# Optimization experiments

Hardware: AMD Instinct MI355X
Metric: run time of the kernel (lower is better)

## Reference

```python
import jax, jax.numpy as jnp
from jax import lax
import numpy as np

B, IMG, PS = 64, 384, 16
DM, DS, DI = 96, 16, 96
DT_RANK = 6
NREP = 4
NCLS = 5
HP = IMG // PS            # 24 patches per side
N = HP * HP               # 576 tokens


def _ln(x, g, b):
    m = x.mean(-1, keepdims=True)
    v = ((x - m) ** 2).mean(-1, keepdims=True)
    return (x - m) * lax.rsqrt(v + 1e-5) * g + b


def setup_inputs() -> dict:
    key = jax.random.key(0)
    ks = jax.random.split(key, 16)
    nrm = lambda k, s: jax.random.normal(k, s, jnp.float32) * 0.02
    return {
        "x": jax.random.uniform(ks[0], (B, 3, IMG, IMG), jnp.float32),
        "W_pe": nrm(ks[1], (DM, 3, PS, PS)), "b_pe": jnp.zeros((DM,), jnp.float32),
        "W_vis": nrm(ks[2], (DM, 1)), "b_vis": jnp.zeros((1,), jnp.float32),
        "dn_g": jnp.ones((DM,), jnp.float32), "dn_b": jnp.zeros((DM,), jnp.float32),
        "W_gate": nrm(ks[3], (DM, DM)), "b_gate": jnp.zeros((DM,), jnp.float32),
        "ln_g": jnp.ones((DM,), jnp.float32), "ln_b": jnp.zeros((DM,), jnp.float32),
        "W_in": nrm(ks[4], (DM, 2 * DI)),
        "conv_w": nrm(ks[5], (DI, 1, 3)),
        "W_xproj": nrm(ks[6], (DI, DT_RANK + 2 * DS)),
        "W_dt": nrm(ks[7], (DT_RANK, DI)), "b_dt": jnp.full((DI,), -2.0, jnp.float32),
        "A_log": jnp.log(jnp.tile(jnp.arange(1, DS + 1, dtype=jnp.float32), (DI, 1))),
        "D": jnp.ones((DI,), jnp.float32),
        "W_out": nrm(ks[8], (DI, DM)),
        "hd_dw": nrm(ks[9], (DM, 1, 3, 3)),
        "bn_g": jnp.ones((DM,), jnp.float32), "bn_b": jnp.zeros((DM,), jnp.float32),
        "bn_m": jnp.zeros((DM,), jnp.float32), "bn_v": jnp.ones((DM,), jnp.float32),
        "W_heat": nrm(ks[10], (NCLS, DM)), "b_heat": jnp.full((NCLS,), -2.19, jnp.float32),
        "W_off": nrm(ks[11], (2, DM)), "b_off": jnp.zeros((2,), jnp.float32),
        "W_size": nrm(ks[12], (2, DM)), "b_size": jnp.zeros((2,), jnp.float32),
    }


def _forward(x, W_pe, b_pe, W_vis, b_vis, dn_g, dn_b, W_gate, b_gate,
             ln_g, ln_b, W_in, conv_w, W_xproj, W_dt, b_dt, A_log, D, W_out,
             hd_dw, bn_g, bn_b, bn_m, bn_v, W_heat, b_heat, W_off, b_off, W_size, b_size):
    # --- retinex preprocessing (single-scale, log domain) ---
    kblur = jnp.ones((3, 1, 5, 5), jnp.float32) / 25.0
    L = lax.conv_general_dilated(x, kblur, (1, 1), 'SAME',
                                 feature_group_count=3,
                                 dimension_numbers=('NCHW', 'OIHW', 'NCHW'))
    x = jnp.log1p(jnp.clip(x, 0.0)) - jnp.log1p(jnp.clip(L, 0.0))
    # --- patch embedding: strided conv -> tokens (B,N,DM) ---
    t = lax.conv_general_dilated(x, W_pe, (PS, PS), 'VALID',
                                 dimension_numbers=('NCHW', 'OIHW', 'NCHW'))
    t = t + b_pe[None, :, None, None]
    tokens = t.reshape(B, DM, N).transpose(0, 2, 1)
    # --- visibility estimator: per-token gate (B,N,1) ---
    vis = jax.nn.sigmoid(tokens @ W_vis + b_vis)
    # --- dual norm: LN + sigmoid gate ---
    tokens = _ln(tokens, dn_g, dn_b)
    norm_gate = jax.nn.sigmoid(tokens @ W_gate + b_gate)  # (B,N,DM)
    # --- weight-shared NC-SSM blocks ---
    A = -jnp.exp(A_log)  # (DI,DS)
    for _ in range(NREP):
        resid = tokens
        h = _ln(tokens, ln_g, ln_b)
        xz = h @ W_in                      # (B,N,2*DI)
        xin, z = xz[..., :DI], xz[..., DI:]
        # causal depthwise conv1d over sequence, kernel 3
        xc = xin.transpose(0, 2, 1)        # (B,DI,N)
        xc = lax.conv_general_dilated(xc, conv_w, (1,), [(2, 0)],
                                      feature_group_count=DI,
                                      dimension_numbers=('NCH', 'OIH', 'NCH'))
        xs = jax.nn.silu(xc.transpose(0, 2, 1))  # (B,N,DI)
        # selective-scan parameters
        proj = xs @ W_xproj                # (B,N,DT_RANK+2*DS)
        dt_raw = proj[..., :DT_RANK]
        Bc = proj[..., DT_RANK:DT_RANK + DS]
        Cc = proj[..., DT_RANK + DS:]
        dt = jax.nn.softplus(dt_raw @ W_dt + b_dt)  # (B,N,DI)
        # time-major scan
        def step(hst, inp):
            dt_t, B_t, C_t, x_t = inp      # (B,DI),(B,DS),(B,DS),(B,DI)
            dA = jnp.exp(dt_t[:, :, None] * A)                 # (B,DI,DS)
            hst = dA * hst + (dt_t * x_t)[:, :, None] * B_t[:, None, :]
            y = jnp.einsum('bds,bs->bd', hst, C_t)
            return hst, y
        h0 = jnp.zeros((B, DI, DS), jnp.float32)
        _, ys = lax.scan(step, h0, (dt.transpose(1, 0, 2), Bc.transpose(1, 0, 2),
                                    Cc.transpose(1, 0, 2), xs.transpose(1, 0, 2)))
        y = ys.transpose(1, 0, 2) + D * xs           # (B,N,DI)
        y = y * jax.nn.silu(z) * vis                  # gated by z and visibility
        tokens = resid + (y @ W_out) * norm_gate
    # --- CenterNet-style head ---
    f = tokens.transpose(0, 2, 1).reshape(B, DM, HP, HP)
    g = lax.conv_general_dilated(f, hd_dw, (1, 1), 'SAME',
                                 feature_group_count=DM,
                                 dimension_numbers=('NCHW', 'OIHW', 'NCHW'))
    g = (g - bn_m[None, :, None, None]) * lax.rsqrt(bn_v + 1e-5)[None, :, None, None]
    g = jax.nn.silu(g * bn_g[None, :, None, None] + bn_b[None, :, None, None])
    heat = jnp.einsum('bchw,oc->bohw', g, W_heat) + b_heat[None, :, None, None]
    off = jnp.einsum('bchw,oc->bohw', f, W_off) + b_off[None, :, None, None]
    size = jnp.einsum('bchw,oc->bohw', f, W_size) + b_size[None, :, None, None]
    return heat, off, size


def reference(x, W_pe, b_pe, W_vis, b_vis, dn_g, dn_b, W_gate, b_gate,
              ln_g, ln_b, W_in, conv_w, W_xproj, W_dt, b_dt, A_log, D, W_out,
              hd_dw, bn_g, bn_b, bn_m, bn_v, W_heat, b_heat, W_off, b_off, W_size, b_size):
    return _forward(x, W_pe, b_pe, W_vis, b_vis, dn_g, dn_b, W_gate, b_gate,
                    ln_g, ln_b, W_in, conv_w, W_xproj, W_dt, b_dt, A_log, D, W_out,
                    hd_dw, bn_g, bn_b, bn_m, bn_v, W_heat, b_heat, W_off, b_off,
                    W_size, b_size)
```

## Files before the change

kernel.cpp:

```cpp
#include <hip/hip_runtime.h>

#define DEVINL __device__ __forceinline__

typedef __attribute__((ext_vector_type(8))) short bf8v;
typedef __attribute__((ext_vector_type(4))) float f4v;

DEVINL float b2f(unsigned short u){ union{unsigned int i; float f;} x; x.i = ((unsigned int)u)<<16; return x.f; }
DEVINL unsigned short f2b(float f){ union{float f; unsigned int i;} x; x.f = f; unsigned int r = x.i + 0x7FFFu + ((x.i>>16)&1u); return (unsigned short)(r>>16); }
DEVINL float sigf(float v){ return 1.f/(1.f + __expf(-v)); }
DEVINL void unpack8(const uint4 u, float* d){
  d[0]=b2f((unsigned short)(u.x)); d[1]=b2f((unsigned short)(u.x>>16));
  d[2]=b2f((unsigned short)(u.y)); d[3]=b2f((unsigned short)(u.y>>16));
  d[4]=b2f((unsigned short)(u.z)); d[5]=b2f((unsigned short)(u.z>>16));
  d[6]=b2f((unsigned short)(u.w)); d[7]=b2f((unsigned short)(u.w>>16));
}
DEVINL uint4 pack8(const float* s){
  uint4 u;
  u.x = (unsigned int)f2b(s[0]) | ((unsigned int)f2b(s[1])<<16);
  u.y = (unsigned int)f2b(s[2]) | ((unsigned int)f2b(s[3])<<16);
  u.z = (unsigned int)f2b(s[4]) | ((unsigned int)f2b(s[5])<<16);
  u.w = (unsigned int)f2b(s[6]) | ((unsigned int)f2b(s[7])<<16);
  return u;
}
union FragU { uint4 u; bf8v v; };


#define PREP_STRIDE (128*256)
__global__ __launch_bounds__(256) void k_prep(
    const float* __restrict__ Wgate, const float* __restrict__ Win,
    const float* __restrict__ Wxproj, const float* __restrict__ Wdt,
    const float* __restrict__ Wout, const float* __restrict__ Alog,
    const float* __restrict__ Wpe, const float* __restrict__ convw,
    unsigned short* __restrict__ WgT, unsigned short* __restrict__ WiT,
    unsigned short* __restrict__ WxT, unsigned short* __restrict__ WoT,
    float* __restrict__ Amat, unsigned short* __restrict__ WpeB,
    float* __restrict__ cwsplit)
{
  int gtid = blockIdx.x*256 + threadIdx.x;
  for (int i = gtid; i < 9216; i += PREP_STRIDE){
    int n = i/96, k = i - n*96;
    WgT[n*96+k] = f2b(Wgate[k*96+n]);
    WoT[n*96+k] = f2b(Wout[k*96+n]);
  }
  for (int i = gtid; i < 18432; i += PREP_STRIDE){
    int n = i/96, k = i - n*96;
    WiT[n*96+k] = f2b(Win[k*192+n]);
  }
  for (int i = gtid; i < 12288; i += PREP_STRIDE){
    int n = i/96, k = i - n*96;
    if (n < 96){
      float s = 0.f;
      for (int r = 0; r < 6; ++r) s += Wxproj[k*38+r] * Wdt[r*96+n];
      WxT[n*96+k] = f2b(s);
    } else {
      WxT[n*96+k] = f2b(Wxproj[k*38 + 6 + (n-96)]);
    }
  }
  for (int i = gtid; i < 1536; i += PREP_STRIDE) Amat[i] = -__expf(Alog[i]);
  for (int i = gtid; i < 73728; i += PREP_STRIDE) WpeB[i] = f2b(Wpe[i]);
  for (int i = gtid; i < 96; i += PREP_STRIDE){
    cwsplit[i]       = convw[i*3+0];
    cwsplit[96+i]    = convw[i*3+1];
    cwsplit[192+i]   = convw[i*3+2];
  }
}

__global__ __launch_bounds__(256) void k_blur(const float* __restrict__ x,
                                              unsigned short* __restrict__ xlog)
{
  __shared__ float xt[12*384];
  __shared__ float vt[8*392];
  int bid = blockIdx.x;
  int tile = bid % 48; int bc = bid / 48; int c = bc % 3; int b = bc / 3;
  const float* xin = x + (size_t)(b*3 + c) * 147456;
  unsigned short* xout = xlog + (size_t)(b*3 + c) * 147456;
  int y0 = tile * 8;
  int tid = threadIdx.x;

  #pragma unroll
  for (int k = 0; k < 5; ++k){
    int idx = tid + k*256;
    if (idx < 1152){
      int r = idx / 96; int c4 = idx - r*96;
      int gy = y0 - 2 + r;
      float4 v = make_float4(0.f,0.f,0.f,0.f);
      if (gy >= 0 && gy < 384) v = *(const float4*)(xin + gy*384 + c4*4);
      *(float4*)(xt + r*384 + c4*4) = v;
    }
  }
  if (tid < 64){
    int r = tid >> 3; int j = tid & 7;
    vt[r*392 + ((j < 4) ? j : (384 + j))] = 0.f;
  }
  __syncthreads();

  #pragma unroll
  for (int k = 0; k < 2; ++k){
    int cc = tid + k*256;
    if (cc < 384){
      float x0 = xt[cc], x1 = xt[384+cc], x2 = xt[768+cc],
            x3 = xt[1152+cc], x4 = xt[1536+cc];
      float vs = ((x0+x1)+(x2+x3))+x4;
      vt[4+cc] = vs;
      #pragma unroll
      for (int r = 1; r < 8; ++r){
        vs += xt[(r+4)*384+cc] - xt[(r-1)*384+cc];
        vt[r*392+4+cc] = vs;
      }
    }
  }
  __syncthreads();

  #pragma unroll
  for (int k = 0; k < 3; ++k){
    int unit = tid + k*256;
    int r = unit / 96; int c4 = unit - r*96;
    int base = r*392 + 4 + c4*4;
    float f[12];
    *(float4*)(f)   = *(const float4*)(vt + base - 4);
    *(float4*)(f+4) = *(const float4*)(vt + base);
    *(float4*)(f+8) = *(const float4*)(vt + base + 4);
    float xv[4];
    *(float4*)(xv) = *(const float4*)(xt + (r+2)*384 + c4*4);
    ushort4 o;
    unsigned short* op = &o.x;
    #pragma unroll
    for (int j = 0; j < 4; ++j){
      float s = f[2+j] + f[3+j] + f[4+j] + f[5+j] + f[6+j];
      float L = fmaxf(s * 0.04f, 0.f);
      float xc = fmaxf(xv[j], 0.f);
      op[j] = f2b(__logf(1.f + xc) - __logf(1.f + L));
    }
    *(ushort4*)(xout + (y0+r)*384 + c4*4) = o;
  }
}

__global__ __launch_bounds__(256) void k_patchln(
    const unsigned short* __restrict__ xlog, const unsigned short* __restrict__ WpeB,
    const float* __restrict__ bpe, const float* __restrict__ dng,
    const float* __restrict__ dnb, const float* __restrict__ Wvis,
    const float* __restrict__ bvis, float* __restrict__ tok, float* __restrict__ vis)
{
  int wid = threadIdx.x >> 6, lane = threadIdx.x & 63;
  int m0 = (blockIdx.x*4 + wid)*16;
  int l15 = lane & 15, q = lane >> 4;
  int ma0 = m0 + l15;
  int b0 = ma0/576; int r0 = ma0 - b0*576; int hp0 = r0/24; int wp0 = r0 - hp0*24;
  size_t base0 = (size_t)b0*442368 + (size_t)hp0*6144 + (size_t)wp0*16;
  f4v acc[6];
  #pragma unroll
  for (int j=0;j<6;++j)
    #pragma unroll
    for (int r=0;r<4;++r) acc[j][r] = 0.f;
  for (int ks = 0; ks < 24; ++ks){
    int k0 = ks*32 + q*8;
    int c  = k0 >> 8;
    int ph = (k0 >> 4) & 15;
    int pw = k0 & 15;
    size_t off = (size_t)c*147456 + (size_t)ph*384 + pw;
    bf8v a0 = *(const bf8v*)(xlog + base0 + off);
    #pragma unroll
    for (int nf = 0; nf < 6; ++nf){
      bf8v bb = *(const bf8v*)(WpeB + (size_t)(nf*16 + l15)*768 + k0);
      acc[nf] = __builtin_amdgcn_mfma_f32_16x16x32_bf16(a0, bb, acc[nf], 0, 0, 0);
    }
  }
  float v[6][4];
  float s[4], w[4], vd[4];
  #pragma unroll
  for (int r=0;r<4;++r){ s[r]=0.f; w[r]=0.f; vd[r]=0.f; }
  #pragma unroll
  for (int nf=0; nf<6; ++nf){
    int n = nf*16 + l15;
    float bp = bpe[n];
    float wv = Wvis[n];
    #pragma unroll
    for (int r=0;r<4;++r){
      float t = acc[nf][r] + bp;
      v[nf][r] = t;
      s[r] += t; w[r] += t*t; vd[r] += t*wv;
    }
  }
  #pragma unroll
  for (int off=1; off<16; off<<=1){
    #pragma unroll
    for (int r=0;r<4;++r){
      s[r]  += __shfl_xor(s[r],  off);
      w[r]  += __shfl_xor(w[r],  off);
      vd[r] += __shfl_xor(vd[r], off);
    }
  }
  float mu[4], rs[4];
  #pragma unroll
  for (int r=0;r<4;++r){
    mu[r] = s[r]*(1.f/96.f);
    rs[r] = rsqrtf(fmaxf(w[r]*(1.f/96.f)-mu[r]*mu[r], 0.f) + 1e-5f);
  }
  if (l15 == 0){
    #pragma unroll
    for (int r=0;r<4;++r) vis[m0 + q*4 + r] = sigf(vd[r] + bvis[0]);
  }
  #pragma unroll
  for (int nf=0; nf<6; ++nf){
    int n = nf*16 + l15;
    float g = dng[n], bb = dnb[n];
    #pragma unroll
    for (int r=0;r<4;++r)
      tok[(size_t)(m0 + q*4 + r)*96 + n] = (v[nf][r]-mu[r])*rs[r]*g + bb;
  }
}

__global__ __launch_bounds__(256) void k_lnfull(const float* __restrict__ tokp,
    const unsigned short* __restrict__ WgT, const float* __restrict__ bg,
    const float* __restrict__ lng, const float* __restrict__ lnb,
    const unsigned short* __restrict__ WiT, const float* __restrict__ vis,
    unsigned short* __restrict__ gate, unsigned short* __restrict__ xin,
    unsigned short* __restrict__ zsv)
{
  int wid = threadIdx.x >> 6, lane = threadIdx.x & 63;
  int gid = blockIdx.x*4 + wid;
  int tile = gid >> 1, half = gid & 1;
  int m0 = tile*16;
  int l15 = lane & 15, q = lane >> 4;
  int ma0 = m0 + l15;
  float a0v[24];
  float s1=0.f, w1=0.f;
  bf8v fa[3];
  #pragma unroll
  for (int ks = 0; ks < 3; ++ks){
    int k0 = ks*32 + q*8;
    float v0[8];
    #pragma unroll
    for (int h = 0; h < 2; ++h){
      float4 va = *(const float4*)(tokp + (size_t)ma0*96 + k0 + h*4);
      int o = ks*8 + h*4;
      a0v[o+0]=va.x; a0v[o+1]=va.y; a0v[o+2]=va.z; a0v[o+3]=va.w;
      v0[h*4+0]=va.x; v0[h*4+1]=va.y; v0[h*4+2]=va.z; v0[h*4+3]=va.w;
      s1 += (va.x+va.y)+(va.z+va.w);
      w1 += (va.x*va.x+va.y*va.y)+(va.z*va.z+va.w*va.w);
    }
    FragU U0; U0.u = pack8(v0);
    fa[ks] = U0.v;
  }
  s1 += __shfl_xor(s1, 16); s1 += __shfl_xor(s1, 32);
  w1 += __shfl_xor(w1, 16); w1 += __shfl_xor(w1, 32);
  float mu1 = s1*(1.f/96.f);
  float rs1 = rsqrtf(fmaxf(w1*(1.f/96.f)-mu1*mu1, 0.f) + 1e-5f);
  bf8v fb[3];
  #pragma unroll
  for (int ks = 0; ks < 3; ++ks){
    int k0 = ks*32 + q*8;
    float gv[8], bv[8];
    *(float4*)(gv)   = *(const float4*)(lng + k0);
    *(float4*)(gv+4) = *(const float4*)(lng + k0 + 4);
    *(float4*)(bv)   = *(const float4*)(lnb + k0);
    *(float4*)(bv+4) = *(const float4*)(lnb + k0 + 4);
    float v0[8];
    #pragma unroll
    for (int j = 0; j < 8; ++j)
      v0[j] = (a0v[ks*8+j]-mu1)*rs1*gv[j] + bv[j];
    FragU U0; U0.u = pack8(v0);
    fb[ks] = U0.v;
  }
  {
    f4v ag[3];
    #pragma unroll
    for (int j=0;j<3;++j)
      #pragma unroll
      for (int r=0;r<4;++r) ag[j][r] = 0.f;
    const bf8v* bpg = (const bf8v*)(WgT) + (size_t)l15*12 + q;
    #pragma unroll
    for (int ks = 0; ks < 3; ++ks)
      #pragma unroll
      for (int nf = 0; nf < 3; ++nf){
        bf8v bb = bpg[(half*3+nf)*192 + ks*4];
        ag[nf] = __builtin_amdgcn_mfma_f32_16x16x32_bf16(fa[ks], bb, ag[nf], 0, 0, 0);
      }
    #pragma unroll
    for (int nf=0; nf<3; ++nf)
      #pragma unroll
      for (int r=0; r<4; ++r){
        int m = m0 + q*4 + r;
        int n = (half*3+nf)*16 + l15;
        gate[(size_t)m*96 + n] = f2b(sigf(ag[nf][r] + bg[n]));
      }
  }
  {
    f4v aw[6];
    #pragma unroll
    for (int j=0;j<6;++j)
      #pragma unroll
      for (int r=0;r<4;++r) aw[j][r] = 0.f;
    const bf8v* bpw = (const bf8v*)(WiT) + (size_t)l15*12 + q;
    #pragma unroll
    for (int ks = 0; ks < 3; ++ks)
      #pragma unroll
      for (int nf = 0; nf < 6; ++nf){
        bf8v bb = bpw[(half*6+nf)*192 + ks*4];
        aw[nf] = __builtin_amdgcn_mfma_f32_16x16x32_bf16(fb[ks], bb, aw[nf], 0, 0, 0);
      }
    if (half == 0){
      #pragma unroll
      for (int nf=0; nf<6; ++nf)
        #pragma unroll
        for (int r=0; r<4; ++r){
          int m = m0 + q*4 + r;
          int n = nf*16 + l15;
          xin[(size_t)m*96 + n] = f2b(aw[nf][r]);
        }
    } else {
      #pragma unroll
      for (int nf=0; nf<6; ++nf)
        #pragma unroll
        for (int r=0; r<4; ++r){
          int m = m0 + q*4 + r;
          int n = nf*16 + l15;
          float v = aw[nf][r];
          float sgl = v * sigf(v);
          zsv[(size_t)m*96 + n] = f2b(sgl * vis[m]);
        }
    }
  }
}

__global__ __launch_bounds__(256) void k_patchfull(
    const unsigned short* __restrict__ xlog, const unsigned short* __restrict__ WpeB,
    const float* __restrict__ bpe,
    const float* __restrict__ dng, const float* __restrict__ dnb,
    const float* __restrict__ Wvis, const float* __restrict__ bvis,
    const unsigned short* __restrict__ WgT, const float* __restrict__ bg,
    const float* __restrict__ lng, const float* __restrict__ lnb,
    const unsigned short* __restrict__ WiT,
    float* __restrict__ tok, unsigned short* __restrict__ gate,
    float* __restrict__ vis, unsigned short* __restrict__ xin,
    unsigned short* __restrict__ zsv)
{
  __shared__ float Sl[2][16][100];
  __shared__ float Vl[2][16];
  int wid = threadIdx.x >> 6, lane = threadIdx.x & 63;
  int gid = blockIdx.x*4 + wid;
  int tile = gid >> 1, half = gid & 1;
  int tl = wid >> 1;
  int m0 = tile*16;
  int l15 = lane & 15, q = lane >> 4;
  int ma0 = m0 + l15;

  {
    int b0 = ma0/576; int r0 = ma0 - b0*576; int hp0 = r0/24; int wp0 = r0 - hp0*24;
    size_t base0 = (size_t)b0*442368 + (size_t)hp0*6144 + (size_t)wp0*16;
    f4v acc[3];
    #pragma unroll
    for (int j=0;j<3;++j)
      #pragma unroll
      for (int r=0;r<4;++r) acc[j][r] = 0.f;
    for (int ks = 0; ks < 24; ++ks){
      int k0 = ks*32 + q*8;
      int c  = k0 >> 8;
      int ph = (k0 >> 4) & 15;
      int pw = k0 & 15;
      size_t off = (size_t)c*147456 + (size_t)ph*384 + pw;
      bf8v a0 = *(const bf8v*)(xlog + base0 + off);
      #pragma unroll
      for (int nf = 0; nf < 3; ++nf){
        bf8v bb = *(const bf8v*)(WpeB + (size_t)((half*3+nf)*16 + l15)*768 + k0);
        acc[nf] = __builtin_amdgcn_mfma_f32_16x16x32_bf16(a0, bb, acc[nf], 0, 0, 0);
      }
    }
    #pragma unroll
    for (int nf=0; nf<3; ++nf)
      #pragma unroll
      for (int r=0; r<4; ++r){
        int n = (half*3+nf)*16 + l15;
        Sl[tl][q*4+r][n] = acc[nf][r] + bpe[n];
      }
  }
  __syncthreads();

  float a0v[24];
  float s0=0.f, w0=0.f, vd=0.f;
  #pragma unroll
  for (int ks = 0; ks < 3; ++ks){
    int k0 = ks*32 + q*8;
    #pragma unroll
    for (int h = 0; h < 2; ++h){
      float4 va = *(const float4*)(&Sl[tl][l15][k0 + h*4]);
      float4 wv = *(const float4*)(Wvis + k0 + h*4);
      int o = ks*8 + h*4;
      a0v[o+0]=va.x; a0v[o+1]=va.y; a0v[o+2]=va.z; a0v[o+3]=va.w;
      s0 += (va.x+va.y)+(va.z+va.w);
      w0 += (va.x*va.x+va.y*va.y)+(va.z*va.z+va.w*va.w);
      vd += (va.x*wv.x+va.y*wv.y)+(va.z*wv.z+va.w*wv.w);
    }
  }
  s0 += __shfl_xor(s0, 16); s0 += __shfl_xor(s0, 32);
  w0 += __shfl_xor(w0, 16); w0 += __shfl_xor(w0, 32);
  vd += __shfl_xor(vd, 16); vd += __shfl_xor(vd, 32);
  float mu0 = s0*(1.f/96.f);
  float rs0 = rsqrtf(fmaxf(w0*(1.f/96.f)-mu0*mu0, 0.f) + 1e-5f);
  if (half == 0 && q == 0){
    float vv = sigf(vd + bvis[0]);
    vis[ma0] = vv;
    Vl[tl][l15] = vv;
  }

  bf8v fa[3];
  float s1=0.f, w1=0.f;
  #pragma unroll
  for (int ks = 0; ks < 3; ++ks){
    int k0 = ks*32 + q*8;
    float gv[8], bv[8];
    *(float4*)(gv)   = *(const float4*)(dng + k0);
    *(float4*)(gv+4) = *(const float4*)(dng + k0 + 4);
    *(float4*)(bv)   = *(const float4*)(dnb + k0);
    *(float4*)(bv+4) = *(const float4*)(dnb + k0 + 4);
    float v0[8];
    #pragma unroll
    for (int j = 0; j < 8; ++j){
      float v = (a0v[ks*8+j]-mu0)*rs0*gv[j] + bv[j];
      v0[j] = v;
      a0v[ks*8+j] = v;
      s1 += v; w1 += v*v;
    }
    if (half == 0){
      *(float4*)(tok + (size_t)ma0*96 + k0)     = make_float4(v0[0],v0[1],v0[2],v0[3]);
      *(float4*)(tok + (size_t)ma0*96 + k0 + 4) = make_float4(v0[4],v0[5],v0[6],v0[7]);
    }
    FragU U0; U0.u = pack8(v0);
    fa[ks] = U0.v;
  }

  {
    f4v ag[3];
    #pragma unroll
    for (int j=0;j<3;++j)
      #pragma unroll
      for (int r=0;r<4;++r) ag[j][r] = 0.f;
    const bf8v* bpg = (const bf8v*)(WgT) + (size_t)l15*12 + q;
    #pragma unroll
    for (int ks = 0; ks < 3; ++ks)
      #pragma unroll
      for (int nf = 0; nf < 3; ++nf){
        bf8v bb = bpg[(half*3+nf)*192 + ks*4];
        ag[nf] = __builtin_amdgcn_mfma_f32_16x16x32_bf16(fa[ks], bb, ag[nf], 0, 0, 0);
      }
    #pragma unroll
    for (int nf=0; nf<3; ++nf)
      #pragma unroll
      for (int r=0; r<4; ++r){
        int m = m0 + q*4 + r;
        int n = (half*3+nf)*16 + l15;
        gate[(size_t)m*96 + n] = f2b(sigf(ag[nf][r] + bg[n]));
      }
  }

  s1 += __shfl_xor(s1, 16); s1 += __shfl_xor(s1, 32);
  w1 += __shfl_xor(w1, 16); w1 += __shfl_xor(w1, 32);
  float mu1 = s1*(1.f/96.f);
  float rs1 = rsqrtf(fmaxf(w1*(1.f/96.f)-mu1*mu1, 0.f) + 1e-5f);
  bf8v fb[3];
  #pragma unroll
  for (int ks = 0; ks < 3; ++ks){
    int k0 = ks*32 + q*8;
    float gv[8], bv[8];
    *(float4*)(gv)   = *(const float4*)(lng + k0);
    *(float4*)(gv+4) = *(const float4*)(lng + k0 + 4);
    *(float4*)(bv)   = *(const float4*)(lnb + k0);
    *(float4*)(bv+4) = *(const float4*)(lnb + k0 + 4);
    float v0[8];
    #pragma unroll
    for (int j = 0; j < 8; ++j)
      v0[j] = (a0v[ks*8+j]-mu1)*rs1*gv[j] + bv[j];
    FragU U0; U0.u = pack8(v0);
    fb[ks] = U0.v;
  }
  __syncthreads();

  {
    f4v aw[6];
    #pragma unroll
    for (int j=0;j<6;++j)
      #pragma unroll
      for (int r=0;r<4;++r) aw[j][r] = 0.f;
    const bf8v* bpw = (const bf8v*)(WiT) + (size_t)l15*12 + q;
    #pragma unroll
    for (int ks = 0; ks < 3; ++ks)
      #pragma unroll
      for (int nf = 0; nf < 6; ++nf){
        bf8v bb = bpw[(half*6+nf)*192 + ks*4];
        aw[nf] = __builtin_amdgcn_mfma_f32_16x16x32_bf16(fb[ks], bb, aw[nf], 0, 0, 0);
      }
    if (half == 0){
      #pragma unroll
      for (int nf=0; nf<6; ++nf)
        #pragma unroll
        for (int r=0; r<4; ++r){
          int m = m0 + q*4 + r;
          int n = nf*16 + l15;
          xin[(size_t)m*96 + n] = f2b(aw[nf][r]);
        }
    } else {
      #pragma unroll
      for (int nf=0; nf<6; ++nf)
        #pragma unroll
        for (int r=0; r<4; ++r){
          int m = m0 + q*4 + r;
          int n = nf*16 + l15;
          float v = aw[nf][r];
          float s = v * sigf(v);
          zsv[(size_t)m*96 + n] = f2b(s * Vl[tl][q*4+r]);
        }
    }
  }
}

template<bool DOLN>
__global__ __launch_bounds__(256) void k_woutln(
    const unsigned short* __restrict__ y2, const unsigned short* __restrict__ WoT,
    const unsigned short* __restrict__ gate,
    const float* __restrict__ lng, const float* __restrict__ lnb,
    const unsigned short* __restrict__ WiT, const float* __restrict__ vis,
    float* __restrict__ tok, unsigned short* __restrict__ xin,
    unsigned short* __restrict__ zsv)
{
  __shared__ float Sl[2][16][100];
  int wid = threadIdx.x >> 6, lane = threadIdx.x & 63;
  int gid = blockIdx.x*4 + wid;
  int tile = gid >> 1, half = gid & 1;
  int tl = wid >> 1;
  int m0 = tile*16;
  int l15 = lane & 15, q = lane >> 4;

  f4v acc[3];
  #pragma unroll
  for (int j=0;j<3;++j)
    #pragma unroll
    for (int r=0;r<4;++r) acc[j][r] = 0.f;
  const bf8v* a0p = (const bf8v*)(y2) + (size_t)(m0 + l15)*12 + q;
  const bf8v* bp  = (const bf8v*)(WoT) + (size_t)l15*12 + q;
  #pragma unroll
  for (int ks = 0; ks < 3; ++ks){
    bf8v a0 = a0p[ks*4];
    #pragma unroll
    for (int nf = 0; nf < 3; ++nf){
      bf8v bb = bp[(half*3+nf)*192 + ks*4];
      acc[nf] = __builtin_amdgcn_mfma_f32_16x16x32_bf16(a0, bb, acc[nf], 0, 0, 0);
    }
  }
  #pragma unroll
  for (int nf=0; nf<3; ++nf)
    #pragma unroll
    for (int r=0; r<4; ++r){
      int m = m0 + q*4 + r;
      int n = (half*3+nf)*16 + l15;
      size_t i = (size_t)m*96 + n;
      float tn = tok[i] + acc[nf][r] * b2f(gate[i]);
      tok[i] = tn;
      if constexpr (DOLN) Sl[tl][q*4+r][n] = tn;
    }

  if constexpr (DOLN){
    __syncthreads();
    int ma0 = m0 + l15;
    float a0v[24];
    float s0=0.f, w0=0.f;
    #pragma unroll
    for (int ks = 0; ks < 3; ++ks){
      int k0 = ks*32 + q*8;
      #pragma unroll
      for (int h = 0; h < 2; ++h){
        float4 va = *(const float4*)(&Sl[tl][l15][k0 + h*4]);
        int o = ks*8 + h*4;
        a0v[o+0]=va.x; a0v[o+1]=va.y; a0v[o+2]=va.z; a0v[o+3]=va.w;
        s0 += (va.x+va.y)+(va.z+va.w);
        w0 += (va.x*va.x+va.y*va.y)+(va.z*va.z+va.w*va.w);
      }
    }
    s0 += __shfl_xor(s0, 16); s0 += __shfl_xor(s0, 32);
    w0 += __shfl_xor(w0, 16); w0 += __shfl_xor(w0, 32);
    float mu0 = s0*(1.f/96.f);
    float rs0 = rsqrtf(fmaxf(w0*(1.f/96.f)-mu0*mu0, 0.f) + 1e-5f);
    bf8v fb[3];
    #pragma unroll
    for (int ks = 0; ks < 3; ++ks){
      int k0 = ks*32 + q*8;
      float gv[8], bv[8];
      *(float4*)(gv)   = *(const float4*)(lng + k0);
      *(float4*)(gv+4) = *(const float4*)(lng + k0 + 4);
      *(float4*)(bv)   = *(const float4*)(lnb + k0);
      *(float4*)(bv+4) = *(const float4*)(lnb + k0 + 4);
      float v0[8];
      #pragma unroll
      for (int j = 0; j < 8; ++j)
        v0[j] = (a0v[ks*8+j]-mu0)*rs0*gv[j] + bv[j];
      FragU U0; U0.u = pack8(v0);
      fb[ks] = U0.v;
    }
    f4v aw[6];
    #pragma unroll
    for (int j=0;j<6;++j)
      #pragma unroll
      for (int r=0;r<4;++r) aw[j][r] = 0.f;
    const bf8v* bpw = (const bf8v*)(WiT) + (size_t)l15*12 + q;
    #pragma unroll
    for (int ks = 0; ks < 3; ++ks)
      #pragma unroll
      for (int nf = 0; nf < 6; ++nf){
        bf8v bb = bpw[(half*6+nf)*192 + ks*4];
        aw[nf] = __builtin_amdgcn_mfma_f32_16x16x32_bf16(fb[ks], bb, aw[nf], 0, 0, 0);
      }
    if (half == 0){
      #pragma unroll
      for (int nf=0; nf<6; ++nf)
        #pragma unroll
        for (int r=0; r<4; ++r){
          int m = m0 + q*4 + r;
          int n = nf*16 + l15;
          xin[(size_t)m*96 + n] = f2b(aw[nf][r]);
        }
    } else {
      #pragma unroll
      for (int nf=0; nf<6; ++nf)
        #pragma unroll
        for (int r=0; r<4; ++r){
          int m = m0 + q*4 + r;
          int n = nf*16 + l15;
          float v = aw[nf][r];
          float sgl = v * sigf(v);
          zsv[(size_t)m*96 + n] = f2b(sgl * vis[m]);
        }
    }
  }
}

__global__ __launch_bounds__(256) void k_convxp(const unsigned short* __restrict__ xinb,
    const float* __restrict__ cwsplit, const unsigned short* __restrict__ BT,
    const float* __restrict__ bdt, unsigned short* __restrict__ xsb,
    unsigned short* __restrict__ dt, unsigned short* __restrict__ bc)
{
  int wid = threadIdx.x >> 6, lane = threadIdx.x & 63;
  int gid = blockIdx.x*4 + wid;
  int tile = gid >> 1, half = gid & 1;
  int m0 = tile*16;
  int nf0 = half*4;
  int l15 = lane & 15, q = lane >> 4;
  int ma0 = m0 + l15;
  int t0 = ma0 % 576;
  const float* cw0 = cwsplit;
  const float* cw1 = cwsplit + 96;
  const float* cw2 = cwsplit + 192;

  bf8v fa0[3];
  uint4 z4 = make_uint4(0,0,0,0);
  #pragma unroll
  for (int ks = 0; ks < 3; ++ks){
    int k0 = ks*32 + q*8;
    const unsigned short* r0p = xinb + (size_t)ma0*96 + k0;
    uint4 c0u  = *(const uint4*)(r0p);
    uint4 p10u = (t0 >= 1) ? *(const uint4*)(r0p - 96)  : z4;
    uint4 p20u = (t0 >= 2) ? *(const uint4*)(r0p - 192) : z4;
    float fc0[8], fp10[8], fp20[8];
    unpack8(c0u, fc0); unpack8(p10u, fp10); unpack8(p20u, fp20);
    float w0v[8], w1v[8], w2v[8];
    *(float4*)(w0v)   = *(const float4*)(cw0 + k0);
    *(float4*)(w0v+4) = *(const float4*)(cw0 + k0 + 4);
    *(float4*)(w1v)   = *(const float4*)(cw1 + k0);
    *(float4*)(w1v+4) = *(const float4*)(cw1 + k0 + 4);
    *(float4*)(w2v)   = *(const float4*)(cw2 + k0);
    *(float4*)(w2v+4) = *(const float4*)(cw2 + k0 + 4);
    float xs0[8];
    #pragma unroll
    for (int j = 0; j < 8; ++j){
      float v0 = w2v[j]*fc0[j] + w1v[j]*fp10[j] + w0v[j]*fp20[j];
      xs0[j] = v0 * sigf(v0);
    }
    FragU U0; U0.u = pack8(xs0);
    fa0[ks] = U0.v;
    if (half == 0) *(uint4*)(xsb + (size_t)ma0*96 + k0) = U0.u;
  }

  f4v acc[4];
  #pragma unroll
  for (int j=0;j<4;++j)
    #pragma unroll
    for (int r=0;r<4;++r) acc[j][r] = 0.f;
  const bf8v* bp = (const bf8v*)(BT) + (size_t)l15*12 + q;
  #pragma unroll
  for (int ks = 0; ks < 3; ++ks){
    #pragma unroll
    for (int nf = 0; nf < 4; ++nf){
      bf8v bb = bp[(nf0+nf)*192 + ks*4];
      acc[nf] = __builtin_amdgcn_mfma_f32_16x16x32_bf16(fa0[ks], bb, acc[nf], 0, 0, 0);
    }
  }
  #pragma unroll
  for (int nf=0; nf<4; ++nf)
    #pragma unroll
    for (int r=0; r<4; ++r){
      int m = m0 + q*4 + r;
      int n = (nf0+nf)*16 + l15;
      float v = acc[nf][r];
      if (n < 96){
        float xx = v + bdt[n];
        float sp = (xx > 20.f) ? xx : __logf(1.f + __expf(xx));
        dt[(size_t)m*96 + n] = f2b(sp);
      } else {
        bc[(size_t)m*32 + (n-96)] = f2b(v);
      }
    }
}

__global__ __launch_bounds__(512) void k_scan(const unsigned short* __restrict__ dt,
    const unsigned short* __restrict__ xsb, const unsigned short* __restrict__ bc,
    const unsigned short* __restrict__ zsv, const float* __restrict__ Amat,
    const float* __restrict__ Dw, unsigned short* __restrict__ y2)
{
  __shared__ float Ul[32*16*17];
  __shared__ float Sl[32*16];
  int b = blockIdx.x / 6; int dg = blockIdx.x - b*6;
  int tid = threadIdx.x;
  int c = tid >> 4; int dl = tid & 15; int d = dg*16 + dl;
  float As[16];
  #pragma unroll
  for (int s = 0; s < 16; s += 4){
    float4 t4 = *(const float4*)(Amat + d*16 + s);
    As[s]=t4.x; As[s+1]=t4.y; As[s+2]=t4.z; As[s+3]=t4.w;
  }
  bool fast = true;
  #pragma unroll
  for (int s = 0; s < 16; ++s)
    fast = fast && (fabsf(As[s] + (float)(s+1)) <= 2e-5f*(float)(s+1));

  float h[16];
  #pragma unroll
  for (int s=0;s<16;++s) h[s]=0.f;
  float sdt = 0.f;
  int tbase = b*576 + c*18;
  if (fast){
    for (int i = 0; i < 18; ++i){
      size_t m = (size_t)(tbase + i);
      float dtv = b2f(dt[m*96 + d]);
      float dtx = dtv * b2f(xsb[m*96 + d]);
      const uint4* bp = (const uint4*)(bc + m*32);
      float Bv[16];
      unpack8(bp[0], Bv); unpack8(bp[1], Bv+8);
      sdt += dtv;
      float w1=__expf(-dtv), w2=w1*w1, w3=w2*w1, w4=w2*w2;
      float w5=w4*w1, w6=w4*w2, w7=w4*w3, w8=w4*w4;
      float w9=w8*w1, w10=w8*w2, w11=w8*w3, w12=w8*w4;
      float w13=w8*w5, w14=w8*w6, w15=w8*w7, w16=w8*w8;
      float dA[16]={w1,w2,w3,w4,w5,w6,w7,w8,w9,w10,w11,w12,w13,w14,w15,w16};
      #pragma unroll
      for (int s=0;s<16;++s) h[s] = dA[s]*h[s] + dtx*Bv[s];
    }
  } else {
    for (int i = 0; i < 18; ++i){
      size_t m = (size_t)(tbase + i);
      float dtv = b2f(dt[m*96 + d]);
      float dtx = dtv * b2f(xsb[m*96 + d]);
      const uint4* bp = (const uint4*)(bc + m*32);
      float Bv[16];
      unpack8(bp[0], Bv); unpack8(bp[1], Bv+8);
      sdt += dtv;
      #pragma unroll
      for (int s=0;s<16;++s) h[s] = __expf(As[s]*dtv)*h[s] + dtx*Bv[s];
    }
  }
  {
    int base = (c*16 + dl)*17;
    #pragma unroll
    for (int s=0;s<16;++s) Ul[base + s] = h[s];
    Sl[c*16 + dl] = sdt;
  }
  __syncthreads();
  if (tid < 256){
    int dl2 = tid >> 4, s2 = tid & 15;
    float A2 = Amat[(dg*16 + dl2)*16 + s2];
    float hh = 0.f;
    for (int cc = 0; cc < 32; ++cc){
      float u = Ul[(cc*16 + dl2)*17 + s2];
      float ss = Sl[cc*16 + dl2];
      hh = __expf(A2*ss)*hh + u;
      Ul[(cc*16 + dl2)*17 + s2] = hh;
    }
  }
  __syncthreads();
  if (c == 0){
    #pragma unroll
    for (int s=0;s<16;++s) h[s] = 0.f;
  } else {
    int base = ((c-1)*16 + dl)*17;
    #pragma unroll
    for (int s=0;s<16;++s) h[s] = Ul[base + s];
  }
  float Dd = Dw[d];
  if (fast){
    for (int i = 0; i < 18; ++i){
      size_t m = (size_t)(tbase + i);
      float dtv = b2f(dt[m*96 + d]);
      float xv = b2f(xsb[m*96 + d]);
      float dtx = dtv * xv;
      const uint4* bp = (const uint4*)(bc + m*32);
      float Bv[16], Cv[16];
      unpack8(bp[0], Bv); unpack8(bp[1], Bv+8);
      unpack8(bp[2], Cv); unpack8(bp[3], Cv+8);
      float w1=__expf(-dtv), w2=w1*w1, w3=w2*w1, w4=w2*w2;
      float w5=w4*w1, w6=w4*w2, w7=w4*w3, w8=w4*w4;
      float w9=w8*w1, w10=w8*w2, w11=w8*w3, w12=w8*w4;
      float w13=w8*w5, w14=w8*w6, w15=w8*w7, w16=w8*w8;
      float dA[16]={w1,w2,w3,w4,w5,w6,w7,w8,w9,w10,w11,w12,w13,w14,w15,w16};
      float p0=0.f,p1=0.f,p2=0.f,p3=0.f;
      #pragma unroll
      for (int s=0;s<16;s+=4){
        h[s+0] = dA[s+0]*h[s+0] + dtx*Bv[s+0]; p0 += h[s+0]*Cv[s+0];
        h[s+1] = dA[s+1]*h[s+1] + dtx*Bv[s+1]; p1 += h[s+1]*Cv[s+1];
        h[s+2] = dA[s+2]*h[s+2] + dtx*Bv[s+2]; p2 += h[s+2]*Cv[s+2];
        h[s+3] = dA[s+3]*h[s+3] + dtx*Bv[s+3]; p3 += h[s+3]*Cv[s+3];
      }
      float y = (p0+p1) + (p2+p3);
      float yv = (y + Dd*xv) * b2f(zsv[m*96 + d]);
      y2[m*96 + d] = f2b(yv);
    }
  } else {
    for (int i = 0; i < 18; ++i){
      size_t m = (size_t)(tbase + i);
      float dtv = b2f(dt[m*96 + d]);
      float xv = b2f(xsb[m*96 + d]);
      float dtx = dtv * xv;
      const uint4* bp = (const uint4*)(bc + m*32);
      float Bv[16], Cv[16];
      unpack8(bp[0], Bv); unpack8(bp[1], Bv+8);
      unpack8(bp[2], Cv); unpack8(bp[3], Cv+8);
      float p0=0.f,p1=0.f,p2=0.f,p3=0.f;
      #pragma unroll
      for (int s=0;s<16;s+=4){
        h[s+0] = __expf(As[s+0]*dtv)*h[s+0] + dtx*Bv[s+0]; p0 += h[s+0]*Cv[s+0];
        h[s+1] = __expf(As[s+1]*dtv)*h[s+1] + dtx*Bv[s+1]; p1 += h[s+1]*Cv[s+1];
        h[s+2] = __expf(As[s+2]*dtv)*h[s+2] + dtx*Bv[s+2]; p2 += h[s+2]*Cv[s+2];
        h[s+3] = __expf(As[s+3]*dtv)*h[s+3] + dtx*Bv[s+3]; p3 += h[s+3]*Cv[s+3];
      }
      float y = (p0+p1) + (p2+p3);
      float yv = (y + Dd*xv) * b2f(zsv[m*96 + d]);
      y2[m*96 + d] = f2b(yv);
    }
  }
}

__global__ __launch_bounds__(256) void k_head(const float* __restrict__ tokens,
    const float* __restrict__ hdw, const float* __restrict__ bng,
    const float* __restrict__ bnb, const float* __restrict__ bnm,
    const float* __restrict__ bnv, const float* __restrict__ Wheat,
    const float* __restrict__ bheat, const float* __restrict__ Woff,
    const float* __restrict__ boff, const float* __restrict__ Wsize,
    const float* __restrict__ bsize, float* __restrict__ out)
{
  __shared__ float ft[3*2304];
  __shared__ float act[2304];
  int b = blockIdx.x / 24; int h = blockIdx.x - b*24;
  for (int i = threadIdx.x; i < 3*2304; i += 256){
    int rr = i / 2304; int j = i - rr*2304;
    int hh = h + rr - 1;
    float v = 0.f;
    if (hh >= 0 && hh < 24) v = tokens[((size_t)b*576 + hh*24)*96 + j];
    ft[rr*2304 + j] = v;
  }
  __syncthreads();
  for (int i = threadIdx.x; i < 2304; i += 256){
    int w = i / 96; int cc = i - w*96;
    float g = 0.f;
    #pragma unroll
    for (int dh = 0; dh < 3; ++dh){
      #pragma unroll
      for (int dw = 0; dw < 3; ++dw){
        int ww = w + dw - 1;
        if (ww >= 0 && ww < 24) g += ft[dh*2304 + ww*96 + cc] * hdw[cc*9 + dh*3 + dw];
      }
    }
    float gn = (g - bnm[cc]) * rsqrtf(bnv[cc] + 1e-5f);
    float a = gn * bng[cc] + bnb[cc];
    act[i] = a * sigf(a);
  }
  __syncthreads();
  int tid = threadIdx.x;
  if (tid < 120){
    int o = tid / 24; int w = tid - o*24;
    float s = 0.f;
    for (int cc = 0; cc < 96; ++cc) s += act[w*96 + cc] * Wheat[o*96 + cc];
    s += bheat[o];
    out[(size_t)b*2880 + o*576 + h*24 + w] = s;
  } else if (tid >= 128 && tid < 224){
    int idx = tid - 128; int o2 = idx / 24; int w = idx - o2*24;
    const float* W = (o2 < 2) ? Woff : Wsize;
    int o = o2 & 1;
    float s = 0.f;
    for (int cc = 0; cc < 96; ++cc) s += ft[2304 + w*96 + cc] * W[o*96 + cc];
    s += ((o2 < 2) ? boff : bsize)[o];
    size_t baseo = (o2 < 2) ? (size_t)184320 : (size_t)258048;
    out[baseo + (size_t)b*1152 + o*576 + h*24 + w] = s;
  }
}

extern "C" void kernel_launch(void* const* d_in, const int* in_sizes, int n_in,
                              void* d_out, int out_size, void* d_ws, size_t ws_size,
                              hipStream_t stream)
{
  (void)in_sizes; (void)n_in; (void)out_size;
  const float* x      = (const float*)d_in[0];
  const float* Wpe    = (const float*)d_in[1];
  const float* bpe    = (const float*)d_in[2];
  const float* Wvis   = (const float*)d_in[3];
  const float* bvis   = (const float*)d_in[4];
  const float* dng    = (const float*)d_in[5];
  const float* dnb    = (const float*)d_in[6];
  const float* Wgate  = (const float*)d_in[7];
  const float* bgate  = (const float*)d_in[8];
  const float* lng    = (const float*)d_in[9];
  const float* lnb    = (const float*)d_in[10];
  const float* Win    = (const float*)d_in[11];
  const float* convw  = (const float*)d_in[12];
  const float* Wxproj = (const float*)d_in[13];
  const float* Wdt    = (const float*)d_in[14];
  const float* bdt    = (const float*)d_in[15];
  const float* Alog   = (const float*)d_in[16];
  const float* Dw     = (const float*)d_in[17];
  const float* Wout   = (const float*)d_in[18];
  const float* hddw   = (const float*)d_in[19];
  const float* bng    = (const float*)d_in[20];
  const float* bnb    = (const float*)d_in[21];
  const float* bnm    = (const float*)d_in[22];
  const float* bnv    = (const float*)d_in[23];
  const float* Wheat  = (const float*)d_in[24];
  const float* bheat  = (const float*)d_in[25];
  const float* Woff   = (const float*)d_in[26];
  const float* boff   = (const float*)d_in[27];
  const float* Wsize  = (const float*)d_in[28];
  const float* bsize  = (const float*)d_in[29];
  float* out = (float*)d_out;

  const bool big = ws_size >= (size_t)120324096;
  char* ws = (char*)d_ws;

  size_t o_xlog = 0;
  size_t o_tok  = 56623104;
  size_t o_vis  = 70778880;
  size_t o_wgt  = 70926336;
  size_t o_wit  = 70944768;
  size_t o_wxt  = 70981632;
  size_t o_wot  = 71006208;
  size_t o_amat = 71024640;
  size_t o_wpe  = 71030784;
  size_t o_cw   = 71178240;
  size_t o_gate, o_xin, o_zsv, o_xsb, o_y2, o_dt, o_bc;
  if (big){
    o_gate = 75497472;  o_xin = 82575360;  o_zsv = 89653248;
    o_xsb  = 96731136;  o_y2  = 103809024; o_dt  = 110886912; o_bc = 117964800;
  } else {
    o_bc   = 0;         o_gate = 14155776; o_xsb = 21233664;
    o_y2   = 28311552;  o_xin  = 35389440; o_zsv = 42467328;  o_dt = 49545216;
  }

  unsigned short* xlog  = (unsigned short*)(ws + o_xlog);
  float*          tok   = (float*)(ws + o_tok);
  float*          vis   = (float*)(ws + o_vis);
  unsigned short* WgT   = (unsigned short*)(ws + o_wgt);
  unsigned short* WiT   = (unsigned short*)(ws + o_wit);
  unsigned short* WxT   = (unsigned short*)(ws + o_wxt);
  unsigned short* WoT   = (unsigned short*)(ws + o_wot);
  float*          Amat  = (float*)(ws + o_amat);
  unsigned short* WpeB  = (unsigned short*)(ws + o_wpe);
  float*          cwsp  = (float*)(ws + o_cw);
  unsigned short* gate  = (unsigned short*)(ws + o_gate);
  unsigned short* xinb  = (unsigned short*)(ws + o_xin);
  unsigned short* zsvb  = (unsigned short*)(ws + o_zsv);
  unsigned short* xsb   = (unsigned short*)(ws + o_xsb);
  unsigned short* y2    = (unsigned short*)(ws + o_y2);
  unsigned short* dtb   = (unsigned short*)(ws + o_dt);
  unsigned short* bcb   = (unsigned short*)(ws + o_bc);

  k_prep<<<128, 256, 0, stream>>>(Wgate, Win, Wxproj, Wdt, Wout, Alog, Wpe, convw,
                                  WgT, WiT, WxT, WoT, Amat, WpeB, cwsp);
  k_blur<<<9216, 256, 0, stream>>>(x, xlog);
  if (big){
    k_patchfull<<<1152, 256, 0, stream>>>(xlog, WpeB, bpe, dng, dnb, Wvis, bvis,
                                          WgT, bgate, lng, lnb, WiT,
                                          tok, gate, vis, xinb, zsvb);
  } else {
    k_patchln<<<576, 256, 0, stream>>>(xlog, WpeB, bpe, dng, dnb, Wvis, bvis, tok, vis);
    k_lnfull<<<1152, 256, 0, stream>>>(tok, WgT, bgate, lng, lnb, WiT, vis,
                                       gate, xinb, zsvb);
  }

  for (int rep = 0; rep < 4; ++rep){
    k_convxp<<<1152, 256, 0, stream>>>(xinb, cwsp, WxT, bdt, xsb, dtb, bcb);
    k_scan<<<384, 512, 0, stream>>>(dtb, xsb, bcb, zsvb, Amat, Dw, y2);
    if (rep < 3)
      k_woutln<true><<<1152, 256, 0, stream>>>(y2, WoT, gate, lng, lnb, WiT, vis,
                                               tok, xinb, zsvb);
    else
      k_woutln<false><<<1152, 256, 0, stream>>>(y2, WoT, gate, lng, lnb, WiT, vis,
                                                tok, xinb, zsvb);
  }

  k_head<<<1536, 256, 0, stream>>>(tok, hddw, bng, bnb, bnm, bnv,
                                   Wheat, bheat, Woff, boff, Wsize, bsize, out);
}
```

Measured before the change: 660.7 us.

## Move SiLU-gate multiply from scan into out-projection and store blur tile as bf16

The multiply of the scan output by the SiLU(z) gate moves out of the serial scan kernel and into the A-operand load of the out-projection GEMM, so the scan no longer reads zsv. Separately, the blur kernel stores the input tile in shared memory as bf16 instead of fp32. Its vertical box sum is recomputed per row with 8-wide vector loads rather than as a running sliding sum. This adds an extra bf16 rounding of the input before the blur and the log, and one more rounding of y before the gate product, both of which can shift accuracy.

```diff
diff --git a/kernel.cpp b/kernel.cpp
--- a/kernel.cpp
+++ b/kernel.cpp
@@ -68,7 +68,7 @@
 __global__ __launch_bounds__(256) void k_blur(const float* __restrict__ x,
                                               unsigned short* __restrict__ xlog)
 {
-  __shared__ float xt[12*384];
+  __shared__ unsigned short xt[12*384];
   __shared__ float vt[8*392];
   int bid = blockIdx.x;
   int tile = bid % 48; int bc = bid / 48; int c = bc % 3; int b = bc / 3;
@@ -85,7 +85,8 @@
       int gy = y0 - 2 + r;
       float4 v = make_float4(0.f,0.f,0.f,0.f);
       if (gy >= 0 && gy < 384) v = *(const float4*)(xin + gy*384 + c4*4);
-      *(float4*)(xt + r*384 + c4*4) = v;
+      ushort4 o; o.x=f2b(v.x); o.y=f2b(v.y); o.z=f2b(v.z); o.w=f2b(v.w);
+      *(ushort4*)(xt + r*384 + c4*4) = o;
     }
   }
   if (tid < 64){
@@ -96,17 +97,23 @@
 
   #pragma unroll
   for (int k = 0; k < 2; ++k){
-    int cc = tid + k*256;
-    if (cc < 384){
-      float x0 = xt[cc], x1 = xt[384+cc], x2 = xt[768+cc],
-            x3 = xt[1152+cc], x4 = xt[1536+cc];
-      float vs = ((x0+x1)+(x2+x3))+x4;
-      vt[4+cc] = vs;
-      #pragma unroll
-      for (int r = 1; r < 8; ++r){
-        vs += xt[(r+4)*384+cc] - xt[(r-1)*384+cc];
-        vt[r*392+4+cc] = vs;
-      }
+    int unit = tid + k*256;
+    if (unit < 384){
+      int r = unit / 48; int c8 = unit - r*48;
+      const unsigned short* base = xt + r*384 + c8*8;
+      float acc[8]; float t[8];
+      uint4 u0 = *(const uint4*)(base);
+      unpack8(u0, acc);
+      #pragma unroll
+      for (int i = 1; i < 5; ++i){
+        uint4 u = *(const uint4*)(base + i*384);
+        unpack8(u, t);
+        #pragma unroll
+        for (int j = 0; j < 8; ++j) acc[j] += t[j];
+      }
+      float* vrow = vt + r*392 + 4 + c8*8;
+      *(float4*)(vrow)   = make_float4(acc[0],acc[1],acc[2],acc[3]);
+      *(float4*)(vrow+4) = make_float4(acc[4],acc[5],acc[6],acc[7]);
     }
   }
   __syncthreads();
@@ -120,16 +127,16 @@
     *(float4*)(f)   = *(const float4*)(vt + base - 4);
     *(float4*)(f+4) = *(const float4*)(vt + base);
     *(float4*)(f+8) = *(const float4*)(vt + base + 4);
-    float xv[4];
-    *(float4*)(xv) = *(const float4*)(xt + (r+2)*384 + c4*4);
+    ushort4 xr = *(const ushort4*)(xt + (r+2)*384 + c4*4);
+    const unsigned short* xrp = &xr.x;
     ushort4 o;
     unsigned short* op = &o.x;
     #pragma unroll
     for (int j = 0; j < 4; ++j){
       float s = f[2+j] + f[3+j] + f[4+j] + f[5+j] + f[6+j];
       float L = fmaxf(s * 0.04f, 0.f);
-      float xc = fmaxf(xv[j], 0.f);
-      op[j] = f2b(__logf(1.f + xc) - __logf(1.f + L));
+      float xv = fmaxf(b2f(xrp[j]), 0.f);
+      op[j] = f2b(__logf(1.f + xv) - __logf(1.f + L));
     }
     *(ushort4*)(xout + (y0+r)*384 + c4*4) = o;
   }
@@ -536,10 +543,18 @@
     #pragma unroll
     for (int r=0;r<4;++r) acc[j][r] = 0.f;
   const bf8v* a0p = (const bf8v*)(y2) + (size_t)(m0 + l15)*12 + q;
+  const bf8v* z0p = (const bf8v*)(zsv) + (size_t)(m0 + l15)*12 + q;
   const bf8v* bp  = (const bf8v*)(WoT) + (size_t)l15*12 + q;
   #pragma unroll
   for (int ks = 0; ks < 3; ++ks){
-    bf8v a0 = a0p[ks*4];
+    FragU Ua, Uz; Ua.v = a0p[ks*4]; Uz.v = z0p[ks*4];
+    float av[8], zv[8];
+    unpack8(Ua.u, av); unpack8(Uz.u, zv);
+    float pv[8];
+    #pragma unroll
+    for (int j = 0; j < 8; ++j) pv[j] = av[j]*zv[j];
+    FragU Up; Up.u = pack8(pv);
+    bf8v a0 = Up.v;
     #pragma unroll
     for (int nf = 0; nf < 3; ++nf){
       bf8v bb = bp[(half*3+nf)*192 + ks*4];
@@ -711,8 +726,8 @@
 
 __global__ __launch_bounds__(512) void k_scan(const unsigned short* __restrict__ dt,
     const unsigned short* __restrict__ xsb, const unsigned short* __restrict__ bc,
-    const unsigned short* __restrict__ zsv, const float* __restrict__ Amat,
-    const float* __restrict__ Dw, unsigned short* __restrict__ y2)
+    const float* __restrict__ Amat, const float* __restrict__ Dw,
+    unsigned short* __restrict__ y2)
 {
   __shared__ float Ul[32*16*17];
   __shared__ float Sl[32*16];
@@ -817,8 +832,7 @@
         h[s+3] = dA[s+3]*h[s+3] + dtx*Bv[s+3]; p3 += h[s+3]*Cv[s+3];
       }
       float y = (p0+p1) + (p2+p3);
-      float yv = (y + Dd*xv) * b2f(zsv[m*96 + d]);
-      y2[m*96 + d] = f2b(yv);
+      y2[m*96 + d] = f2b(y + Dd*xv);
     }
   } else {
     for (int i = 0; i < 18; ++i){
@@ -839,8 +853,7 @@
         h[s+3] = __expf(As[s+3]*dtv)*h[s+3] + dtx*Bv[s+3]; p3 += h[s+3]*Cv[s+3];
       }
       float y = (p0+p1) + (p2+p3);
-      float yv = (y + Dd*xv) * b2f(zsv[m*96 + d]);
-      y2[m*96 + d] = f2b(yv);
+      y2[m*96 + d] = f2b(y + Dd*xv);
     }
   }
 }
@@ -991,7 +1004,7 @@
 
   for (int rep = 0; rep < 4; ++rep){
     k_convxp<<<1152, 256, 0, stream>>>(xinb, cwsp, WxT, bdt, xsb, dtb, bcb);
-    k_scan<<<384, 512, 0, stream>>>(dtb, xsb, bcb, zsvb, Amat, Dw, y2);
+    k_scan<<<384, 512, 0, stream>>>(dtb, xsb, bcb, Amat, Dw, y2);
     if (rep < 3)
       k_woutln<true><<<1152, 256, 0, stream>>>(y2, WoT, gate, lng, lnb, WiT, vis,
                                                tok, xinb, zsvb);
```

Measured after the change: 656.6 us (median of 2 runs). About the same (-0.6%).
